# Kernel tuning notes

Hardware: AMD Instinct MI355X
Metric: run time of the kernel (lower is better)

The kernel has to match this reference:

```python
import jax, jax.numpy as jnp
import numpy as np

K = 9            # connections per output pixel
GA = 2           # global additional samples
RA = 2           # relative additional samples
VS = 4 + GA + RA # 2^rank neighbours + sampled
REGION = 12      # int(0.25 * 48) per spatial dim
MMULT = 0.1
MIN_SIGMA = 0.05
SIGMA_SCALE = 0.05
SIGMA_BOOST = 2.0


def setup_inputs() -> dict:
    key = jax.random.key(0)
    ks = jax.random.split(key, 8)
    b, cin, h, w = 8, 128, 48, 48
    cout = 256
    hidden = cin * 4

    def lin_init(k, fan_out, fan_in):
        bound = 1.0 / np.sqrt(fan_in)
        kw, kb = jax.random.split(k)
        W = jax.random.uniform(kw, (fan_out, fan_in), minval=-bound, maxval=bound, dtype=jnp.float32)
        bb = jax.random.uniform(kb, (fan_out,), minval=-bound, maxval=bound, dtype=jnp.float32)
        return W, bb

    x = jax.random.normal(ks[0], (b, cin, h, w), dtype=jnp.float32)
    W1, b1 = lin_init(ks[1], hidden, 2)          # toparams layer 1 (adaptive=False -> 2 coord inputs)
    W2, b2 = lin_init(ks[2], 3 * K, hidden)      # toparams layer 2 -> k means (2d) + k sigmas
    Wu, bu = lin_init(ks[3], cout, K * cin)      # unify linear
    gints = jax.random.randint(ks[4], (b, h, w, K, GA, 2), 0, h, dtype=jnp.int32)      # global samples (h==w)
    roff = jax.random.randint(ks[5], (b, h, w, K, RA, 2), 0, REGION, dtype=jnp.int32)  # relative offsets
    return {"x": x, "W1": W1, "b1": b1, "W2": W2, "b2": b2, "Wu": Wu, "bu": bu,
            "gints": gints, "roff": roff}


def reference(x, W1, b1, W2, b2, Wu, bu, gints, roff):
    b, c, h, w = x.shape
    s = jnp.array([h, w], dtype=x.dtype)                       # spatial range per dim
    s_int = jnp.array([h, w], dtype=jnp.int32)

    # normalized coordinate grid in [0,1], (h, w, 2) with [.,.,0]=row, [.,.,1]=col
    rows = jnp.arange(h, dtype=x.dtype) / (h - 1)
    cols = jnp.arange(w, dtype=x.dtype) / (w - 1)
    coords = jnp.stack(jnp.meshgrid(rows, cols, indexing='ij'), axis=-1)

    # hypernetwork: per-pixel coords -> K 2d mean offsets + K sigmas
    inp = jnp.broadcast_to(coords, (b, h, w, 2))
    hid = jax.nn.relu(inp @ W1.T + b1)
    params = hid @ W2.T + b2                                   # (b,h,w,3K)
    means_raw = params[..., :2 * K].reshape(b, h, w, K, 2)
    sig_raw = params[..., 2 * K:]                              # (b,h,w,K)

    # mids: inverse of the sigmoid scaling applied to the pixel's own coordinate
    pix = coords * (s - 1)                                     # pixel coordinates
    sc = pix / (s - 1) * 0.9999 + 0.00005
    mids = jnp.log(sc / (1.0 - sc))                            # (h,w,2)

    # transform_means: sigmoid -> [0, s-1]
    means = jax.nn.sigmoid(mids[None, :, :, None, :] + MMULT * means_raw) * (s - 1)  # (b,h,w,K,2)
    # transform_sigmas: softplus(. + boost) + min, per-dim scale, then sigma_scale
    sigmas = (jax.nn.softplus(sig_raw + SIGMA_BOOST) + MIN_SIGMA)[..., None] * s * SIGMA_SCALE  # (b,h,w,K,2)

    # ---- integer index generation (non-differentiable) ----
    fl = jnp.floor(jax.lax.stop_gradient(means)).astype(jnp.int32)   # (b,h,w,K,2)
    combos = jnp.array([[0, 0], [0, 1], [1, 0], [1, 1]], dtype=jnp.int32)
    neigh = fl[..., None, :] + combos                                 # (b,h,w,K,4,2)
    rel = fl[..., None, :] + roff - REGION // 2                       # (b,h,w,K,RA,2)
    ints = jnp.concatenate([neigh, gints, rel], axis=-2) % s_int      # (b,h,w,K,VS,2)

    # duplicate masking: zero any tuple that occurred earlier along VS
    eq = jnp.all(ints[..., :, None, :] == ints[..., None, :, :], axis=-1)  # (...,VS,VS)
    lower = jnp.tril(jnp.ones((VS, VS), dtype=bool), k=-1)
    dups = jnp.any(eq & lower, axis=-1)                               # (b,h,w,K,VS)

    # unnormalized gaussian densities of integer points under (means, sigmas)
    diff = (ints.astype(x.dtype) - means[..., None, :]) / sigmas[..., None, :]
    props = jnp.exp(-0.5 * jnp.sum(diff * diff, axis=-1))             # (b,h,w,K,VS)
    props = jnp.where(dups, jnp.zeros((), x.dtype), props)
    weights = props / jnp.sum(props, axis=-1, keepdims=True)          # mvalues are all-ones

    # irregular gather of input channel vectors at sampled pixels
    lin = ints[..., 0] * w + ints[..., 1]                             # (b,h,w,K,VS)
    flat = x.transpose(0, 2, 3, 1).reshape(b, h * w, c)
    feats = flat[jnp.arange(b)[:, None], lin.reshape(b, -1)]          # (b, h*w*K*VS, c)
    feats = feats.reshape(b, h, w, K, VS, c)

    feats = jnp.einsum('bhwkvc,bhwkv->bhwkc', feats, weights)         # weighted reduce over VS
    feats = feats.reshape(b, h, w, K * c)
    out = feats @ Wu.T + bu                                           # unify linear
    return out.transpose(0, 3, 1, 2)                                  # (b, cout, h, w)
```

## Files before the change

kernel.cpp:

```cpp
#include <hip/hip_runtime.h>
#include <hip/hip_bf16.h>
#include <hip/hip_fp16.h>

#define BB 8
#define CIN 128
#define HH 48
#define WW 48
#define HW 2304
#define KK 9
#define COUT 256
#define KC 1152
#define MM 18432
#define MT 16
#define SFP 136

#define LIGHT_BARRIER() asm volatile("s_waitcnt lgkmcnt(0)\n\ts_barrier" ::: "memory")

typedef short bf16x8_t __attribute__((ext_vector_type(8)));
typedef float f32x4_t  __attribute__((ext_vector_type(4)));

static __device__ __forceinline__ float b2f(short u) {
    union { unsigned int i; float f; } c;
    c.i = ((unsigned int)(unsigned short)u) << 16;
    return c.f;
}

__global__ __launch_bounds__(256) void prep_kernel(
    const float* __restrict__ x, __hip_bfloat16* __restrict__ xT,
    const float* __restrict__ Wu, bf16x8_t* __restrict__ Bp,
    const float* __restrict__ W1, const float* __restrict__ b1,
    const float* __restrict__ W2, const float* __restrict__ b2,
    float* __restrict__ means, float* __restrict__ sigmas, int* __restrict__ fls)
{
    __shared__ double s_par[4][27];
    int bid = blockIdx.x;
    int t = threadIdx.x;

    if (bid < 576) {
        __shared__ float tile[64][65];
        int ij0 = (bid % 36) * 64;
        int c0  = ((bid / 36) % 2) * 64;
        int b   = bid / 72;
        int ijl = t & 63, cl = t >> 6;
        #pragma unroll
        for (int i = 0; i < 16; i++) {
            int cc = i*4 + cl;
            tile[cc][ijl] = x[(size_t)(b*CIN + c0 + cc) * HW + ij0 + ijl];
        }
        __syncthreads();
        int cl2 = t & 63, ijl2 = t >> 6;
        #pragma unroll
        for (int i = 0; i < 16; i++) {
            int ij = i*4 + ijl2;
            xT[(size_t)(b*HW + ij0 + ij) * CIN + c0 + cl2] = __float2bfloat16(tile[cl2][ij]);
        }
    } else if (bid < 720) {
        int idx = (bid - 576) * 256 + t;
        int lane = idx & 63;
        int rest = idx >> 6;
        int ksub = rest % 36, tile16 = rest / 36;
        const float* src = Wu + (size_t)(tile16*16 + (lane & 15)) * KC
                              + ksub*32 + (lane >> 4)*8;
        union { bf16x8_t v; __hip_bfloat16 h[8]; } o;
        #pragma unroll
        for (int j = 0; j < 8; j++) o.h[j] = __float2bfloat16(src[j]);
        Bp[idx] = o.v;
    } else {
        int wave = t >> 6, lane = t & 63;
        int p = (bid - 720) * 4 + wave;
        int iy = p / WW, ix = p % WW;
        float ryf = (float)iy / 47.0f;
        float rxf = (float)ix / 47.0f;
        double ry = (double)ryf, rx = (double)rxf;

        double h[8];
        #pragma unroll
        for (int jj = 0; jj < 8; jj++) {
            int j = lane*8 + jj;
            double v = ry * (double)W1[j*2+0] + rx * (double)W1[j*2+1] + (double)b1[j];
            h[jj] = v > 0.0 ? v : 0.0;
        }
        for (int g = 0; g < 3; g++) {
            double par[9];
            #pragma unroll
            for (int oo = 0; oo < 9; oo++) {
                int o = g*9 + oo;
                const float4* w4 = (const float4*)(W2 + (size_t)o*512 + lane*8);
                float4 wa = w4[0], wb = w4[1];
                double s = (double)wa.x*h[0] + (double)wa.y*h[1]
                         + (double)wa.z*h[2] + (double)wa.w*h[3]
                         + (double)wb.x*h[4] + (double)wb.y*h[5]
                         + (double)wb.z*h[6] + (double)wb.w*h[7];
                par[oo] = s;
            }
            #pragma unroll
            for (int oo = 0; oo < 9; oo++) {
                #pragma unroll
                for (int d = 1; d < 64; d <<= 1)
                    par[oo] += __shfl_xor(par[oo], d, 64);
            }
            if (lane == 0) {
                #pragma unroll
                for (int oo = 0; oo < 9; oo++)
                    s_par[wave][g*9 + oo] = par[oo] + (double)b2[g*9 + oo];
            }
        }
        __syncthreads();
        if (lane < KK) {
            int k = lane;
            double scy = ry * 0.9999 + 5e-05;
            double scx = rx * 0.9999 + 5e-05;
            double midy = log(scy / (1.0 - scy));
            double midx = log(scx / (1.0 - scx));
            double zy = midy + 0.1 * s_par[wave][2*k+0];
            double zx = midx + 0.1 * s_par[wave][2*k+1];
            double my = 47.0 / (1.0 + exp(-zy));
            double mx = 47.0 / (1.0 + exp(-zx));
            double sr = s_par[wave][18 + k] + 2.0;
            double sp = (sr > 0.0 ? sr : 0.0) + log1p(exp(-fabs(sr)));
            double sg = (sp + 0.05) * 48.0 * 0.05;
            means[(p*KK + k)*2 + 0] = (float)my;
            means[(p*KK + k)*2 + 1] = (float)mx;
            sigmas[p*KK + k] = (float)sg;
            fls[(p*KK + k)*2 + 0] = (int)floor(my);
            fls[(p*KK + k)*2 + 1] = (int)floor(mx);
        }
    }
}

__global__ __launch_bounds__(256, 3) void fused_kernel(
    const float* __restrict__ means, const float* __restrict__ sigmas,
    const int* __restrict__ fls, const int* __restrict__ gints,
    const int* __restrict__ roff, const short* __restrict__ xT,
    const bf16x8_t* __restrict__ Bp, const float* __restrict__ bu,
    float* __restrict__ out)
{
    __shared__ unsigned int s_tap[KK*MT*8];
    __shared__ __align__(16) short s_feat[KK][MT*SFP];

    int t = threadIdx.x;
    int b   = blockIdx.x & 7;
    int grp = blockIdx.x >> 3;
    int ij0 = grp * MT;
    int m0  = b * HW + ij0;

    if (t < KK*MT) {
        int p = t;
        int k = p >> 4, row = p & 15;
        int ij = ij0 + row;
        int bij = m0 + row;
        int fy = fls[(ij*KK + k)*2 + 0];
        int fx = fls[(ij*KK + k)*2 + 1];
        float my = means[(ij*KK + k)*2 + 0];
        float mx = means[(ij*KK + k)*2 + 1];
        float sg = sigmas[ij*KK + k];
        int lins[8]; float ws[8];
        #pragma unroll
        for (int v = 0; v < 8; v++) {
            int iy, ix;
            if (v < 4) {
                iy = fy + (v >> 1); ix = fx + (v & 1);
            } else if (v < 6) {
                int base = ((bij*KK + k)*2 + (v - 4)) * 2;
                iy = gints[base]; ix = gints[base + 1];
            } else {
                int base = ((bij*KK + k)*2 + (v - 6)) * 2;
                iy = fy + roff[base] - 6; ix = fx + roff[base + 1] - 6;
            }
            iy = ((iy % HH) + HH) % HH;
            ix = ((ix % WW) + WW) % WW;
            lins[v] = iy * WW + ix;
            float dy = ((float)iy - my) / sg;
            float dx = ((float)ix - mx) / sg;
            ws[v] = expf(-0.5f * (dy*dy + dx*dx));
        }
        #pragma unroll
        for (int v = 1; v < 8; v++) {
            bool dup = false;
            #pragma unroll
            for (int u = 0; u < 8; u++) if (u < v) dup = dup || (lins[u] == lins[v]);
            if (dup) ws[v] = 0.0f;
        }
        float sum = 0.0f;
        #pragma unroll
        for (int v = 0; v < 8; v++) sum += ws[v];
        float inv = 1.0f / sum;
        #pragma unroll
        for (int v = 0; v < 8; v++) {
            unsigned short hb = __half_as_ushort(__float2half(ws[v] * inv));
            s_tap[p*8+v] = ((unsigned int)lins[v] << 16) | (unsigned int)hb;
        }
    }
    LIGHT_BARRIER();

    const short* xb = xT + (size_t)b * (HW * CIN);
    int lane = t & 63, wave = t >> 6;
    int grow = t >> 4, gc0 = (t & 15) << 3;
    int arow = lane & 15, aq = lane >> 4;

    {
        bf16x8_t tap[8];
        float    wgt[8];
        {
            const unsigned int* tp = &s_tap[(0*MT + grow)*8];
            #pragma unroll
            for (int v = 0; v < 8; v++) {
                unsigned int e = tp[v];
                wgt[v] = __half2float(__ushort_as_half((unsigned short)(e & 0xffffu)));
                tap[v] = *(const bf16x8_t*)(xb + (size_t)(e >> 16) * CIN + gc0);
            }
        }
        for (int k = 0; k < KK; k++) {
            float a0[8];
            #pragma unroll
            for (int j = 0; j < 8; j++) a0[j] = 0.0f;
            #pragma unroll
            for (int v = 0; v < 8; v++) {
                float w = wgt[v]; bf16x8_t d8 = tap[v];
                #pragma unroll
                for (int j = 0; j < 8; j++) a0[j] += w * b2f(d8[j]);
            }
            if (k < KK - 1) {
                const unsigned int* tp = &s_tap[((k+1)*MT + grow)*8];
                #pragma unroll
                for (int v = 0; v < 8; v++) {
                    unsigned int e = tp[v];
                    wgt[v] = __half2float(__ushort_as_half((unsigned short)(e & 0xffffu)));
                    tap[v] = *(const bf16x8_t*)(xb + (size_t)(e >> 16) * CIN + gc0);
                }
            }
            union { bf16x8_t v8; __hip_bfloat16 hh[8]; } o;
            #pragma unroll
            for (int j = 0; j < 8; j++) o.hh[j] = __float2bfloat16(a0[j]);
            *(bf16x8_t*)(&s_feat[k][grow*SFP + gc0]) = o.v8;
        }
    }
    LIGHT_BARRIER();
    f32x4_t acc[4] = {};
    for (int k = 0; k < KK; k++) {
        bf16x8_t Bf[16];
        {
            int base = (wave*4*36 + k*4)*64 + lane;
            #pragma unroll
            for (int tl = 0; tl < 4; tl++)
                #pragma unroll
                for (int s4 = 0; s4 < 4; s4++)
                    Bf[tl*4 + s4] = Bp[base + (tl*36 + s4)*64];
        }
        const short* fb = s_feat[k];
        bf16x8_t av[4];
        #pragma unroll
        for (int s4 = 0; s4 < 4; s4++)
            av[s4] = *(const bf16x8_t*)(fb + arow*SFP + s4*32 + aq*8);
        #pragma unroll
        for (int tl = 0; tl < 4; tl++)
            #pragma unroll
            for (int s4 = 0; s4 < 4; s4++)
                acc[tl] = __builtin_amdgcn_mfma_f32_16x16x32_bf16(av[s4], Bf[tl*4 + s4], acc[tl], 0, 0, 0);
    }

    #pragma unroll
    for (int tl = 0; tl < 4; tl++) {
        int n = (wave*4 + tl)*16 + arow;
        float bv = bu[n];
        f32x4_t vv;
        vv[0] = acc[tl][0] + bv;
        vv[1] = acc[tl][1] + bv;
        vv[2] = acc[tl][2] + bv;
        vv[3] = acc[tl][3] + bv;
        *(f32x4_t*)(out + ((size_t)b * COUT + n) * HW + ij0 + aq*4) = vv;
    }
}

extern "C" void kernel_launch(void* const* d_in, const int* in_sizes, int n_in,
                              void* d_out, int out_size, void* d_ws, size_t ws_size,
                              hipStream_t stream)
{
    const float* x   = (const float*)d_in[0];
    const float* W1  = (const float*)d_in[1];
    const float* b1  = (const float*)d_in[2];
    const float* W2  = (const float*)d_in[3];
    const float* b2  = (const float*)d_in[4];
    const float* Wu  = (const float*)d_in[5];
    const float* bu  = (const float*)d_in[6];
    const int* gints = (const int*)d_in[7];
    const int* roff  = (const int*)d_in[8];
    float* out = (float*)d_out;

    char* ws = (char*)d_ws;
    float* ws_means  = (float*)(ws + 0);
    float* ws_sigma  = (float*)(ws + 165888);
    int*   ws_fl     = (int*  )(ws + 248832);
    short* ws_xT     = (short*)(ws + 414720);
    bf16x8_t* ws_bp  = (bf16x8_t*)(ws + 5133312);

    prep_kernel<<<1296, 256, 0, stream>>>(x, (__hip_bfloat16*)ws_xT, Wu, ws_bp,
                                          W1, b1, W2, b2,
                                          ws_means, ws_sigma, ws_fl);
    fused_kernel<<<MM/MT, 256, 0, stream>>>(ws_means, ws_sigma, ws_fl, gints, roff,
                                            ws_xT, ws_bp, bu, out);
}
```

Baseline: 144.7 us.

## Split gather and MFMA phases into two halves to shrink LDS and raise occupancy

The kernel now computes the weighted-gather features for taps 0-4, runs the MFMA accumulation over them, then reuses the same shared buffer for taps 5-8. This cuts the s_feat shared array from 9 to 5 slices, and launch_bounds now asks for 6 blocks per CU instead of 3. The aim is more resident blocks to hide gather latency. The cost is an extra barrier, and the compiler may have to limit registers to meet the tighter occupancy target, which could cause spills.

```diff
diff --git a/kernel.cpp b/kernel.cpp
--- a/kernel.cpp
+++ b/kernel.cpp
@@ -128,7 +128,7 @@
     }
 }
 
-__global__ __launch_bounds__(256, 3) void fused_kernel(
+__global__ __launch_bounds__(256, 6) void fused_kernel(
     const float* __restrict__ means, const float* __restrict__ sigmas,
     const int* __restrict__ fls, const int* __restrict__ gints,
     const int* __restrict__ roff, const short* __restrict__ xT,
@@ -136,7 +136,7 @@
     float* __restrict__ out)
 {
     __shared__ unsigned int s_tap[KK*MT*8];
-    __shared__ __align__(16) short s_feat[KK][MT*SFP];
+    __shared__ __align__(16) short s_feat[5][MT*SFP];
 
     int t = threadIdx.x;
     int b   = blockIdx.x & 7;
@@ -198,11 +198,31 @@
     int grow = t >> 4, gc0 = (t & 15) << 3;
     int arow = lane & 15, aq = lane >> 4;
 
+    f32x4_t acc[4] = {};
+    bf16x8_t tap[8];
+    float    wgt[8];
     {
-        bf16x8_t tap[8];
-        float    wgt[8];
+        const unsigned int* tp = &s_tap[(0*MT + grow)*8];
+        #pragma unroll
+        for (int v = 0; v < 8; v++) {
+            unsigned int e = tp[v];
+            wgt[v] = __half2float(__ushort_as_half((unsigned short)(e & 0xffffu)));
+            tap[v] = *(const bf16x8_t*)(xb + (size_t)(e >> 16) * CIN + gc0);
+        }
+    }
+
+    for (int k = 0; k < 5; k++) {
+        float a0[8];
+        #pragma unroll
+        for (int j = 0; j < 8; j++) a0[j] = 0.0f;
+        #pragma unroll
+        for (int v = 0; v < 8; v++) {
+            float w = wgt[v]; bf16x8_t d8 = tap[v];
+            #pragma unroll
+            for (int j = 0; j < 8; j++) a0[j] += w * b2f(d8[j]);
+        }
         {
-            const unsigned int* tp = &s_tap[(0*MT + grow)*8];
+            const unsigned int* tp = &s_tap[((k+1)*MT + grow)*8];
             #pragma unroll
             for (int v = 0; v < 8; v++) {
                 unsigned int e = tp[v];
@@ -210,34 +230,13 @@
                 tap[v] = *(const bf16x8_t*)(xb + (size_t)(e >> 16) * CIN + gc0);
             }
         }
-        for (int k = 0; k < KK; k++) {
-            float a0[8];
-            #pragma unroll
-            for (int j = 0; j < 8; j++) a0[j] = 0.0f;
-            #pragma unroll
-            for (int v = 0; v < 8; v++) {
-                float w = wgt[v]; bf16x8_t d8 = tap[v];
-                #pragma unroll
-                for (int j = 0; j < 8; j++) a0[j] += w * b2f(d8[j]);
-            }
-            if (k < KK - 1) {
-                const unsigned int* tp = &s_tap[((k+1)*MT + grow)*8];
-                #pragma unroll
-                for (int v = 0; v < 8; v++) {
-                    unsigned int e = tp[v];
-                    wgt[v] = __half2float(__ushort_as_half((unsigned short)(e & 0xffffu)));
-                    tap[v] = *(const bf16x8_t*)(xb + (size_t)(e >> 16) * CIN + gc0);
-                }
-            }
-            union { bf16x8_t v8; __hip_bfloat16 hh[8]; } o;
-            #pragma unroll
-            for (int j = 0; j < 8; j++) o.hh[j] = __float2bfloat16(a0[j]);
-            *(bf16x8_t*)(&s_feat[k][grow*SFP + gc0]) = o.v8;
-        }
+        union { bf16x8_t v8; __hip_bfloat16 hh[8]; } o;
+        #pragma unroll
+        for (int j = 0; j < 8; j++) o.hh[j] = __float2bfloat16(a0[j]);
+        *(bf16x8_t*)(&s_feat[k][grow*SFP + gc0]) = o.v8;
     }
     LIGHT_BARRIER();
-    f32x4_t acc[4] = {};
-    for (int k = 0; k < KK; k++) {
+    for (int k = 0; k < 5; k++) {
         bf16x8_t Bf[16];
         {
             int base = (wave*4*36 + k*4)*64 + lane;
@@ -248,6 +247,53 @@
                     Bf[tl*4 + s4] = Bp[base + (tl*36 + s4)*64];
         }
         const short* fb = s_feat[k];
+        bf16x8_t av[4];
+        #pragma unroll
+        for (int s4 = 0; s4 < 4; s4++)
+            av[s4] = *(const bf16x8_t*)(fb + arow*SFP + s4*32 + aq*8);
+        #pragma unroll
+        for (int tl = 0; tl < 4; tl++)
+            #pragma unroll
+            for (int s4 = 0; s4 < 4; s4++)
+                acc[tl] = __builtin_amdgcn_mfma_f32_16x16x32_bf16(av[s4], Bf[tl*4 + s4], acc[tl], 0, 0, 0);
+    }
+    LIGHT_BARRIER();
+    for (int k = 5; k < KK; k++) {
+        float a0[8];
+        #pragma unroll
+        for (int j = 0; j < 8; j++) a0[j] = 0.0f;
+        #pragma unroll
+        for (int v = 0; v < 8; v++) {
+            float w = wgt[v]; bf16x8_t d8 = tap[v];
+            #pragma unroll
+            for (int j = 0; j < 8; j++) a0[j] += w * b2f(d8[j]);
+        }
+        if (k < KK - 1) {
+            const unsigned int* tp = &s_tap[((k+1)*MT + grow)*8];
+            #pragma unroll
+            for (int v = 0; v < 8; v++) {
+                unsigned int e = tp[v];
+                wgt[v] = __half2float(__ushort_as_half((unsigned short)(e & 0xffffu)));
+                tap[v] = *(const bf16x8_t*)(xb + (size_t)(e >> 16) * CIN + gc0);
+            }
+        }
+        union { bf16x8_t v8; __hip_bfloat16 hh[8]; } o;
+        #pragma unroll
+        for (int j = 0; j < 8; j++) o.hh[j] = __float2bfloat16(a0[j]);
+        *(bf16x8_t*)(&s_feat[k-5][grow*SFP + gc0]) = o.v8;
+    }
+    LIGHT_BARRIER();
+    for (int k = 5; k < KK; k++) {
+        bf16x8_t Bf[16];
+        {
+            int base = (wave*4*36 + k*4)*64 + lane;
+            #pragma unroll
+            for (int tl = 0; tl < 4; tl++)
+                #pragma unroll
+                for (int s4 = 0; s4 < 4; s4++)
+                    Bf[tl*4 + s4] = Bp[base + (tl*36 + s4)*64];
+        }
+        const short* fb = s_feat[k-5];
         bf16x8_t av[4];
         #pragma unroll
         for (int s4 = 0; s4 < 4; s4++)
```

Measured after the change: 173.4 us. +19.8%, slower.

## Split gather/MFMA into two phases with double-buffered taps and B fragments

Applied to the files above, without the earlier changes.

Restructures the fused kernel into two phases (taps 0-4, then 5-8), so the feature staging buffer in shared memory drops from 9 to 5 slots and occupancy is raised to 4 blocks per CU. Gather loads are double-buffered across two register sets to keep more global loads in flight. B-fragment loads for the MFMA loop are split in halves and software-pipelined against the MFMAs. This adds an extra barrier and more live registers, which may cause spills under the tighter launch bound.

```diff
diff --git a/kernel.cpp b/kernel.cpp
--- a/kernel.cpp
+++ b/kernel.cpp
@@ -128,7 +128,54 @@
     }
 }
 
-__global__ __launch_bounds__(256, 3) void fused_kernel(
+#define TAP_LOAD(TP, WG, kk) do {                                             \
+    const unsigned int* _tp = &s_tap[((kk)*MT + grow)*8];                     \
+    _Pragma("unroll")                                                         \
+    for (int v = 0; v < 8; v++) {                                             \
+        unsigned int e = _tp[v];                                              \
+        WG[v] = __half2float(__ushort_as_half((unsigned short)(e & 0xffffu)));\
+        TP[v] = *(const bf16x8_t*)(xb + (size_t)(e >> 16) * CIN + gc0);       \
+    } } while (0)
+
+#define TAP_MATH(TP, WG, slot) do {                                           \
+    float a0[8];                                                              \
+    _Pragma("unroll") for (int j = 0; j < 8; j++) a0[j] = 0.0f;               \
+    _Pragma("unroll")                                                         \
+    for (int v = 0; v < 8; v++) {                                             \
+        float w = WG[v]; bf16x8_t d8 = TP[v];                                 \
+        _Pragma("unroll") for (int j = 0; j < 8; j++) a0[j] += w * b2f(d8[j]);\
+    }                                                                         \
+    union { bf16x8_t v8; __hip_bfloat16 hh[8]; } o;                           \
+    _Pragma("unroll") for (int j = 0; j < 8; j++) o.hh[j] = __float2bfloat16(a0[j]); \
+    *(bf16x8_t*)(&s_feat[slot][grow*SFP + gc0]) = o.v8;                       \
+    } while (0)
+
+#define BF_LOAD(BF, kk, hh) do {                                              \
+    int _base = (wave*4*36 + (kk)*4)*64 + lane;                               \
+    _Pragma("unroll")                                                         \
+    for (int tl2 = 0; tl2 < 2; tl2++)                                         \
+        _Pragma("unroll")                                                     \
+        for (int s4 = 0; s4 < 4; s4++)                                        \
+            BF[tl2*4 + s4] = Bp[_base + (((hh)*2 + tl2)*36 + s4)*64];         \
+    } while (0)
+
+#define HALF_MFMA(BF, hh) do {                                                \
+    _Pragma("unroll")                                                         \
+    for (int tl2 = 0; tl2 < 2; tl2++)                                         \
+        _Pragma("unroll")                                                     \
+        for (int s4 = 0; s4 < 4; s4++)                                        \
+            acc[(hh)*2 + tl2] = __builtin_amdgcn_mfma_f32_16x16x32_bf16(      \
+                av[s4], BF[tl2*4 + s4], acc[(hh)*2 + tl2], 0, 0, 0);          \
+    } while (0)
+
+#define AV_LOAD(slot) do {                                                    \
+    const short* _fb = s_feat[slot];                                          \
+    _Pragma("unroll")                                                         \
+    for (int s4 = 0; s4 < 4; s4++)                                            \
+        av[s4] = *(const bf16x8_t*)(_fb + arow*SFP + s4*32 + aq*8);           \
+    } while (0)
+
+__global__ __launch_bounds__(256, 4) void fused_kernel(
     const float* __restrict__ means, const float* __restrict__ sigmas,
     const int* __restrict__ fls, const int* __restrict__ gints,
     const int* __restrict__ roff, const short* __restrict__ xT,
@@ -136,7 +183,7 @@
     float* __restrict__ out)
 {
     __shared__ unsigned int s_tap[KK*MT*8];
-    __shared__ __align__(16) short s_feat[KK][MT*SFP];
+    __shared__ __align__(16) short s_feat[5][MT*SFP];
 
     int t = threadIdx.x;
     int b   = blockIdx.x & 7;
@@ -198,65 +245,57 @@
     int grow = t >> 4, gc0 = (t & 15) << 3;
     int arow = lane & 15, aq = lane >> 4;
 
+    f32x4_t acc[4] = {};
+    bf16x8_t tapA[8], tapB[8];
+    float    wgtA[8], wgtB[8];
+
+    TAP_LOAD(tapA, wgtA, 0);
+    TAP_LOAD(tapB, wgtB, 1);
+    TAP_MATH(tapA, wgtA, 0);
+    TAP_LOAD(tapA, wgtA, 2);
+    TAP_MATH(tapB, wgtB, 1);
+    TAP_LOAD(tapB, wgtB, 3);
+    TAP_MATH(tapA, wgtA, 2);
+    TAP_LOAD(tapA, wgtA, 4);
+    TAP_MATH(tapB, wgtB, 3);
+    TAP_MATH(tapA, wgtA, 4);
+    LIGHT_BARRIER();
+
     {
-        bf16x8_t tap[8];
-        float    wgt[8];
-        {
-            const unsigned int* tp = &s_tap[(0*MT + grow)*8];
-            #pragma unroll
-            for (int v = 0; v < 8; v++) {
-                unsigned int e = tp[v];
-                wgt[v] = __half2float(__ushort_as_half((unsigned short)(e & 0xffffu)));
-                tap[v] = *(const bf16x8_t*)(xb + (size_t)(e >> 16) * CIN + gc0);
-            }
-        }
-        for (int k = 0; k < KK; k++) {
-            float a0[8];
-            #pragma unroll
-            for (int j = 0; j < 8; j++) a0[j] = 0.0f;
-            #pragma unroll
-            for (int v = 0; v < 8; v++) {
-                float w = wgt[v]; bf16x8_t d8 = tap[v];
-                #pragma unroll
-                for (int j = 0; j < 8; j++) a0[j] += w * b2f(d8[j]);
-            }
-            if (k < KK - 1) {
-                const unsigned int* tp = &s_tap[((k+1)*MT + grow)*8];
-                #pragma unroll
-                for (int v = 0; v < 8; v++) {
-                    unsigned int e = tp[v];
-                    wgt[v] = __half2float(__ushort_as_half((unsigned short)(e & 0xffffu)));
-                    tap[v] = *(const bf16x8_t*)(xb + (size_t)(e >> 16) * CIN + gc0);
-                }
-            }
-            union { bf16x8_t v8; __hip_bfloat16 hh[8]; } o;
-            #pragma unroll
-            for (int j = 0; j < 8; j++) o.hh[j] = __float2bfloat16(a0[j]);
-            *(bf16x8_t*)(&s_feat[k][grow*SFP + gc0]) = o.v8;
+        bf16x8_t BfA[8], BfB[8], av[4];
+        BF_LOAD(BfA, 0, 0);
+        #pragma unroll
+        for (int k = 0; k < 5; k++) {
+            AV_LOAD(k);
+            BF_LOAD(BfB, k, 1);
+            HALF_MFMA(BfA, 0);
+            if (k < 4) BF_LOAD(BfA, k+1, 0);
+            HALF_MFMA(BfB, 1);
         }
     }
     LIGHT_BARRIER();
-    f32x4_t acc[4] = {};
-    for (int k = 0; k < KK; k++) {
-        bf16x8_t Bf[16];
-        {
-            int base = (wave*4*36 + k*4)*64 + lane;
-            #pragma unroll
-            for (int tl = 0; tl < 4; tl++)
-                #pragma unroll
-                for (int s4 = 0; s4 < 4; s4++)
-                    Bf[tl*4 + s4] = Bp[base + (tl*36 + s4)*64];
-        }
-        const short* fb = s_feat[k];
-        bf16x8_t av[4];
-        #pragma unroll
-        for (int s4 = 0; s4 < 4; s4++)
-            av[s4] = *(const bf16x8_t*)(fb + arow*SFP + s4*32 + aq*8);
-        #pragma unroll
-        for (int tl = 0; tl < 4; tl++)
-            #pragma unroll
-            for (int s4 = 0; s4 < 4; s4++)
-                acc[tl] = __builtin_amdgcn_mfma_f32_16x16x32_bf16(av[s4], Bf[tl*4 + s4], acc[tl], 0, 0, 0);
+
+    TAP_LOAD(tapB, wgtB, 5);
+    TAP_LOAD(tapA, wgtA, 6);
+    TAP_MATH(tapB, wgtB, 0);
+    TAP_LOAD(tapB, wgtB, 7);
+    TAP_MATH(tapA, wgtA, 1);
+    TAP_LOAD(tapA, wgtA, 8);
+    TAP_MATH(tapB, wgtB, 2);
+    TAP_MATH(tapA, wgtA, 3);
+    LIGHT_BARRIER();
+
+    {
+        bf16x8_t BfA[8], BfB[8], av[4];
+        BF_LOAD(BfA, 5, 0);
+        #pragma unroll
+        for (int k = 5; k < KK; k++) {
+            AV_LOAD(k-5);
+            BF_LOAD(BfB, k, 1);
+            HALF_MFMA(BfA, 0);
+            if (k < KK-1) BF_LOAD(BfA, k+1, 0);
+            HALF_MFMA(BfB, 1);
+        }
     }
 
     #pragma unroll
```

After: 144.4 us. No clear change (-0.2%).
